# Optimization experiments

Measured on AMD Instinct MI355X. Metric: run time of the kernel, lower is better.

## Reference

```python
import jax, jax.numpy as jnp
import numpy as np

R = 2          # total_rel
N = 6144       # total_ent / num nodes
H1 = 256       # layer 1 out
H2 = 256       # layer 2 out


def setup_inputs() -> dict:
    key = jax.random.key(0)
    k_adj, k_w1, k_c1, k_w2, k_c2 = jax.random.split(key, 5)
    adj = jax.random.uniform(k_adj, (R, N, N), dtype=jnp.float32)
    bw1 = jax.random.normal(k_w1, (R, N, H1), dtype=jnp.float32) * (1.0 / np.sqrt(N))
    bc1 = jax.random.normal(k_c1, (R, R), dtype=jnp.float32)
    bw2 = jax.random.normal(k_w2, (R, H1, H2), dtype=jnp.float32) * (1.0 / np.sqrt(H1))
    bc2 = jax.random.normal(k_c2, (R, R), dtype=jnp.float32)
    return {"adj": adj, "bw1": bw1, "bc1": bc1, "bw2": bw2, "bc2": bc2}


def _layer_weights(coeff, basis):
    # (R, n_basis) x (n_basis, in, out) -> (R*in, out)
    w = jnp.einsum('ij,jmn->imn', coeff, basis)
    return w.reshape(w.shape[0] * w.shape[1], w.shape[2])


def reference(adj, bw1, bc1, bw2, bc2):
    # --- layer 1: node_init is None -> features are dense adjacencies ---
    w1 = _layer_weights(bc1, bw1)                        # (R*N, H1)
    # cat([adj[0], adj[1]], axis=1) == transpose+reshape  (N, R*N)
    tmp1 = adj.transpose(1, 0, 2).reshape(N, R * N)
    out1 = tmp1 @ w1                                     # (N, H1)

    # --- layer 2: relu then per-relation spmm + basis matmul ---
    x = jax.nn.relu(out1)
    w2 = _layer_weights(bc2, bw2)                        # (R*H1, H2)
    # cat([adj[r] @ x for r], axis=1) as one einsum       (N, R*H1)
    tmp2 = jnp.einsum('rij,jd->ird', adj, x).reshape(N, R * H1)
    out2 = tmp2 @ w2                                     # (N, H2)

    final_rep = jnp.concatenate([out1, out2], axis=1)    # (N, H1+H2)
    final_rep = jnp.sum(final_rep, axis=0).reshape(-1, H1 + H2)  # (1, H1+H2)
    return (out2, final_rep)
```

## Files before the change

### kernel.cpp

```cpp
#include <hip/hip_runtime.h>


#define NN 6144
#define HH 256
#define SPLIT 8
#define KCHUNK 1536
#define KSTEPS 24

typedef __attribute__((ext_vector_type(4))) float f32x4;
typedef __attribute__((ext_vector_type(8))) unsigned short u16x8;
typedef __attribute__((ext_vector_type(4))) unsigned short u16x4;

__device__ __forceinline__ unsigned short f2bf(float f) {
  unsigned int u = __float_as_uint(f);
  u += 0x7FFFu + ((u >> 16) & 1u);
  return (unsigned short)(u >> 16);
}
__device__ __forceinline__ float bf2f(unsigned short h) {
  return __uint_as_float(((unsigned int)h) << 16);
}

__device__ __forceinline__ void mfma_bf16(f32x4& d, u16x8 a, u16x8 b) {
  asm("v_mfma_f32_16x16x32_bf16 %0, %1, %2, %0" : "+v"(d) : "v"(a), "v"(b));
}

#define BAR_PRE_STAGE()   asm volatile("s_barrier" ::: "memory")
#define BAR_PRE_COMPUTE() asm volatile("s_waitcnt lgkmcnt(0)\n\ts_barrier" ::: "memory")

__global__ void prep_kernel(const float* __restrict__ bw1, const float* __restrict__ bc1,
                            const float* __restrict__ bw2, const float* __restrict__ bc2,
                            unsigned short* __restrict__ B1ws, unsigned short* __restrict__ w2ws,
                            float* __restrict__ fin)
{
  const int b   = blockIdx.x;
  const int tid = threadIdx.x;
  if (b >= 200) { fin[(b - 200) * 256 + tid] = 0.f; return; }

  const float* basis; const float* bc; unsigned short* outw;
  int tilesPerR, jdim, t;
  if (b < 192) { basis = bw1; bc = bc1; outw = B1ws; tilesPerR = 96; jdim = NN; t = b; }
  else         { basis = bw2; bc = bc2; outw = w2ws; tilesPerR = 4;  jdim = HH; t = b - 192; }

  __shared__ unsigned short wt[64][265];
  const int r  = t / tilesPerR;
  const int jt = t % tilesPerR;
  const float c0 = bc[r * 2 + 0];
  const float c1 = bc[r * 2 + 1];
  const float* b0 = basis + (size_t)jt * 64 * HH;
  const float* b1 = basis + (size_t)jdim * HH + (size_t)jt * 64 * HH;
#pragma unroll
  for (int k = 0; k < 16; ++k) {
    int idx = tid + k * 256;
    int row = idx >> 6;
    int c4  = (idx & 63) * 4;
    f32x4 v0 = *(const f32x4*)(b0 + (size_t)row * HH + c4);
    f32x4 v1 = *(const f32x4*)(b1 + (size_t)row * HH + c4);
    wt[row][c4 + 0] = f2bf(c0 * v0.x + c1 * v1.x);
    wt[row][c4 + 1] = f2bf(c0 * v0.y + c1 * v1.y);
    wt[row][c4 + 2] = f2bf(c0 * v0.z + c1 * v1.z);
    wt[row][c4 + 3] = f2bf(c0 * v0.w + c1 * v1.w);
  }
  __syncthreads();
#pragma unroll
  for (int k = 0; k < 8; ++k) {
    int chunk = tid + k * 256;
    int h  = chunk >> 3;
    int sp = chunk & 7;
    int j0 = (sp ^ (h & 7)) * 8;
    u16x8 v;
#pragma unroll
    for (int e = 0; e < 8; ++e) v[e] = wt[j0 + e][h];
    *(u16x8*)(outw + ((size_t)t * 2048 + chunk) * 8) = v;
  }
}

#define GEMM_PROLOGUE_COMMON()                                                 \
  const int tid  = threadIdx.x;                                                \
  const int lane = tid & 63;                                                   \
  const int wave = tid >> 6;                                                   \
  const int bid  = blockIdx.x;                                                 \
  const int s    = bid & 7;                    \
  const int mb   = bid >> 3;                                                   \
  const int i0 = mb * 64;                                                      \
  const int kbase = s * KCHUNK;                                                \
  const int tBase = kbase / 64;                                                \
  const unsigned short* bBase = Bws + (size_t)tBase * 2048 * 8 + (size_t)tid * 8;

#define DECL_ACC()                                                             \
  f32x4 acc[4][4];                                                             \
  _Pragma("unroll")                                                            \
  for (int m = 0; m < 4; ++m)                                                  \
    _Pragma("unroll")                                                          \
    for (int n = 0; n < 4; ++n) acc[m][n] = (f32x4){0.f, 0.f, 0.f, 0.f};

#define ISSUE_B(KK) do {                                                       \
    _Pragma("unroll")                                                          \
    for (int c = 0; c < 8; ++c)                                                \
      bv[c] = *(const u16x8*)(bBase + (size_t)(KK) * 2048 * 8 + c * 256 * 8);  \
  } while (0)

#define STAGE_B() do {                                                         \
    _Pragma("unroll")                                                          \
    for (int c = 0; c < 8; ++c)                                                \
      *(u16x8*)(Blds + ((size_t)c * 256 + tid) * 8) = bv[c];                   \
  } while (0)

#define COMPUTE() do {                                                         \
    _Pragma("unroll")                                                          \
    for (int ks = 0; ks < 2; ++ks) {                                           \
      u16x8 af[4], bfr[4];                                                     \
      _Pragma("unroll")                                                        \
      for (int m = 0; m < 4; ++m) {                                            \
        int row = m * 16 + (lane & 15);                                        \
        int off = (ks * 64 + ((lane >> 4) << 4)) ^ ((row & 7) << 4);           \
        af[m] = *(const u16x8*)((const char*)Alds + row * 128 + off);          \
      }                                                                        \
      _Pragma("unroll")                                                        \
      for (int n = 0; n < 4; ++n) {                                            \
        int row = wave * 64 + n * 16 + (lane & 15);                            \
        int off = (ks * 64 + ((lane >> 4) << 4)) ^ ((row & 7) << 4);           \
        bfr[n] = *(const u16x8*)((const char*)Blds + row * 128 + off);         \
      }                                                                        \
      _Pragma("unroll")                                                        \
      for (int m = 0; m < 4; ++m)                                              \
        _Pragma("unroll")                                                      \
        for (int n = 0; n < 4; ++n)                                            \
          mfma_bf16(acc[m][n], af[m], bfr[n]);                                 \
    } } while (0)

#define WRITE_P() do {                                                         \
    unsigned short* P = Pp + ((size_t)s * NN + i0) * HH;                       \
    _Pragma("unroll")                                                          \
    for (int m = 0; m < 4; ++m)                                                \
      _Pragma("unroll")                                                        \
      for (int n = 0; n < 4; ++n) {                                            \
        int col = wave * 64 + n * 16 + (lane & 15);                            \
        _Pragma("unroll")                                                      \
        for (int q = 0; q < 4; ++q) {                                          \
          int row = m * 16 + ((lane >> 4) << 2) + q;                           \
          P[(size_t)row * HH + col] = f2bf(acc[m][n][q]);                      \
        }                                                                      \
      } } while (0)

#define ISSUE_A(SET, KK) do {                                                  \
    _Pragma("unroll")                                                          \
    for (int it = 0; it < 4; ++it)                                             \
      SET[it] = *(const f32x4*)(aRow + (size_t)it * 16 * NN + (KK) * 64);      \
  } while (0)

__global__ __launch_bounds__(256, 3) void gemm_adj_store_kernel(
    const float* __restrict__ adj, const unsigned short* __restrict__ Bws,
    unsigned short* __restrict__ Pp, unsigned short* __restrict__ Aws)
{
  __shared__ __align__(16) unsigned short Alds[64 * 64];
  __shared__ __align__(16) unsigned short Blds[256 * 64];
  GEMM_PROLOGUE_COMMON();
  const int rrel = kbase / NN;
  const int jb   = kbase % NN;
  const float* aRow = adj + (size_t)rrel * NN * NN
                      + (size_t)(i0 + (tid >> 4)) * NN + jb + (tid & 15) * 4;
  char* aTile0 = (char*)Aws + ((size_t)(s * 96 + mb) * 24) * 8192;

  DECL_ACC();
  f32x4 av0[4], av1[4];
  u16x8 bv[8];

#define STAGE_A_ST(SET, KK) do {                                               \
    char* at = aTile0 + (size_t)(KK) * 8192;                                   \
    _Pragma("unroll")                                                          \
    for (int it = 0; it < 4; ++it) {                                           \
      int row = (tid >> 4) + it * 16;                                          \
      int off = ((tid & 15) * 8) ^ ((row & 7) << 4);                           \
      u16x4 w;                                                                 \
      w[0] = f2bf(SET[it].x); w[1] = f2bf(SET[it].y);                          \
      w[2] = f2bf(SET[it].z); w[3] = f2bf(SET[it].w);                          \
      *(u16x4*)((char*)Alds + row * 128 + off) = w;                            \
      *(u16x4*)(at + row * 128 + off) = w;                                     \
    } } while (0)

  ISSUE_A(av0, 0);
  ISSUE_A(av1, 1);
  ISSUE_B(0);

  for (int kk = 0; kk < KSTEPS; kk += 2) {
    BAR_PRE_STAGE();
    STAGE_A_ST(av0, kk);
    STAGE_B();
    BAR_PRE_COMPUTE();
    ISSUE_B(kk + 1);
    COMPUTE();
    BAR_PRE_STAGE();
    STAGE_A_ST(av1, kk + 1);
    STAGE_B();
    BAR_PRE_COMPUTE();
    if (kk + 2 < KSTEPS) {
      ISSUE_A(av0, kk + 2);
      ISSUE_A(av1, kk + 3);
      ISSUE_B(kk + 2);
    }
    COMPUTE();
  }
#undef STAGE_A_ST
  WRITE_P();
}

__global__ __launch_bounds__(256, 3) void gemm_adj_bf_kernel(
    const unsigned short* __restrict__ Aws, const unsigned short* __restrict__ Bws,
    unsigned short* __restrict__ Pp)
{
  __shared__ __align__(16) unsigned short Alds[64 * 64];
  __shared__ __align__(16) unsigned short Blds[256 * 64];
  GEMM_PROLOGUE_COMMON();
  const char* aTile0 = (const char*)Aws + ((size_t)(s * 96 + mb) * 24) * 8192;

  DECL_ACC();
  u16x8 av0[2], av1[2];
  u16x8 bv[8];

#define ISSUE_A2(SET, KK) do {                                                 \
    const char* at = aTile0 + (size_t)(KK) * 8192 + (size_t)tid * 32;          \
    SET[0] = *(const u16x8*)(at);                                              \
    SET[1] = *(const u16x8*)(at + 16);                                         \
  } while (0)

#define STAGE_A2(SET) do {                                                     \
    *(u16x8*)((char*)Alds + (size_t)tid * 32) = SET[0];                        \
    *(u16x8*)((char*)Alds + (size_t)tid * 32 + 16) = SET[1];                   \
  } while (0)

  ISSUE_A2(av0, 0);
  ISSUE_A2(av1, 1);
  ISSUE_B(0);

  for (int kk = 0; kk < KSTEPS; kk += 2) {
    BAR_PRE_STAGE();
    STAGE_A2(av0);
    STAGE_B();
    BAR_PRE_COMPUTE();
    ISSUE_B(kk + 1);
    COMPUTE();
    BAR_PRE_STAGE();
    STAGE_A2(av1);
    STAGE_B();
    BAR_PRE_COMPUTE();
    if (kk + 2 < KSTEPS) {
      ISSUE_A2(av0, kk + 2);
      ISSUE_A2(av1, kk + 3);
      ISSUE_B(kk + 2);
    }
    COMPUTE();
  }
#undef ISSUE_A2
#undef STAGE_A2
  WRITE_P();
}

__global__ __launch_bounds__(256, 3) void gemm_adj_kernel(
    const float* __restrict__ adj, const unsigned short* __restrict__ Bws,
    unsigned short* __restrict__ Pp)
{
  __shared__ __align__(16) unsigned short Alds[64 * 64];
  __shared__ __align__(16) unsigned short Blds[256 * 64];
  GEMM_PROLOGUE_COMMON();
  const int rrel = kbase / NN;
  const int jb   = kbase % NN;
  const float* aRow = adj + (size_t)rrel * NN * NN
                      + (size_t)(i0 + (tid >> 4)) * NN + jb + (tid & 15) * 4;

  DECL_ACC();
  f32x4 av0[4], av1[4];
  u16x8 bv[8];

#define STAGE_A(SET) do {                                                      \
    _Pragma("unroll")                                                          \
    for (int it = 0; it < 4; ++it) {                                           \
      int row = (tid >> 4) + it * 16;                                          \
      int off = ((tid & 15) * 8) ^ ((row & 7) << 4);                           \
      u16x4 w;                                                                 \
      w[0] = f2bf(SET[it].x); w[1] = f2bf(SET[it].y);                          \
      w[2] = f2bf(SET[it].z); w[3] = f2bf(SET[it].w);                          \
      *(u16x4*)((char*)Alds + row * 128 + off) = w;                            \
    } } while (0)

  ISSUE_A(av0, 0);
  ISSUE_A(av1, 1);
  ISSUE_B(0);

  for (int kk = 0; kk < KSTEPS; kk += 2) {
    BAR_PRE_STAGE();
    STAGE_A(av0);
    STAGE_B();
    BAR_PRE_COMPUTE();
    ISSUE_B(kk + 1);
    COMPUTE();
    BAR_PRE_STAGE();
    STAGE_A(av1);
    STAGE_B();
    BAR_PRE_COMPUTE();
    if (kk + 2 < KSTEPS) {
      ISSUE_A(av0, kk + 2);
      ISSUE_A(av1, kk + 3);
      ISSUE_B(kk + 2);
    }
    COMPUTE();
  }
#undef STAGE_A
  WRITE_P();
}

__global__ __launch_bounds__(256, 2) void gemm_y_kernel(
    const unsigned short* __restrict__ xws, const unsigned short* __restrict__ w2ws,
    unsigned short* __restrict__ B2ws)
{
  __shared__ __align__(16) unsigned short Alds[64 * 64];
  __shared__ __align__(16) unsigned short Blds[256 * 64];
  const int tid  = threadIdx.x;
  const int lane = tid & 63;
  const int wave = tid >> 6;
  const int mb = blockIdx.x;
  const int r  = blockIdx.y;

  f32x4 acc[4][4];
#pragma unroll
  for (int m = 0; m < 4; ++m)
#pragma unroll
    for (int n = 0; n < 4; ++n) acc[m][n] = (f32x4){0.f, 0.f, 0.f, 0.f};

  for (int dt = 0; dt < 4; ++dt) {
    u16x8 avv[2];
    avv[0] = *(const u16x8*)(xws + (((size_t)(mb * 4 + dt)) * 512 + tid) * 8);
    avv[1] = *(const u16x8*)(xws + (((size_t)(mb * 4 + dt)) * 512 + 256 + tid) * 8);
    u16x8 bv[8];
#pragma unroll
    for (int c = 0; c < 8; ++c)
      bv[c] = *(const u16x8*)(w2ws + (((size_t)(r * 4 + dt)) * 2048 + c * 256 + tid) * 8);
    __syncthreads();
    *(u16x8*)(Alds + (size_t)tid * 8) = avv[0];
    *(u16x8*)(Alds + ((size_t)256 + tid) * 8) = avv[1];
#pragma unroll
    for (int c = 0; c < 8; ++c)
      *(u16x8*)(Blds + ((size_t)c * 256 + tid) * 8) = bv[c];
    __syncthreads();
#pragma unroll
    for (int ks = 0; ks < 2; ++ks) {
      u16x8 af[4], bfr[4];
#pragma unroll
      for (int m = 0; m < 4; ++m) {
        int row = m * 16 + (lane & 15);
        int off = (ks * 64 + ((lane >> 4) << 4)) ^ ((row & 7) << 4);
        af[m] = *(const u16x8*)((const char*)Alds + row * 128 + off);
      }
#pragma unroll
      for (int n = 0; n < 4; ++n) {
        int row = wave * 64 + n * 16 + (lane & 15);
        int off = (ks * 64 + ((lane >> 4) << 4)) ^ ((row & 7) << 4);
        bfr[n] = *(const u16x8*)((const char*)Blds + row * 128 + off);
      }
#pragma unroll
      for (int m = 0; m < 4; ++m)
#pragma unroll
        for (int n = 0; n < 4; ++n)
          mfma_bf16(acc[m][n], af[m], bfr[n]);
    }
  }
  const int tg = r * 96 + mb;
#pragma unroll
  for (int m = 0; m < 4; ++m) {
    int scont = m * 2 + ((lane >> 4) >> 1);
    int e0    = ((lane >> 4) & 1) * 4;
#pragma unroll
    for (int n = 0; n < 4; ++n) {
      int h   = wave * 64 + n * 16 + (lane & 15);
      int pos = scont ^ (h & 7);
      u16x4 v;
      v[0] = f2bf(acc[m][n][0]); v[1] = f2bf(acc[m][n][1]);
      v[2] = f2bf(acc[m][n][2]); v[3] = f2bf(acc[m][n][3]);
      *(u16x4*)(B2ws + (((size_t)tg * 2048 + h * 8 + pos) * 8 + e0)) = v;
    }
  }
}

__global__ void reduce1_kernel(const unsigned short* __restrict__ Pp,
                               unsigned short* __restrict__ xws,
                               float* __restrict__ fin)
{
  __shared__ float csm[8][256];
  const int tid = threadIdx.x;
  const int b   = blockIdx.x;
  const int hc  = tid & 31;
  const int rg  = tid >> 5;
  const int dt    = hc >> 3;
  const int scont = hc & 7;
  float cs[8] = {0.f, 0.f, 0.f, 0.f, 0.f, 0.f, 0.f, 0.f};
  for (int k = 0; k < 8; ++k) {
    int i = b * 64 + rg + k * 8;
    float sv[8] = {0.f, 0.f, 0.f, 0.f, 0.f, 0.f, 0.f, 0.f};
#pragma unroll
    for (int s = 0; s < SPLIT; ++s) {
      u16x8 v = *(const u16x8*)(Pp + ((size_t)s * NN + i) * HH + hc * 8);
#pragma unroll
      for (int e = 0; e < 8; ++e) sv[e] += bf2f(v[e]);
    }
    u16x8 xv;
#pragma unroll
    for (int e = 0; e < 8; ++e) {
      cs[e] += sv[e];
      xv[e] = f2bf(fmaxf(sv[e], 0.f));
    }
    int pos = scont ^ (i & 7);
    *(u16x8*)(xws + (((size_t)(b * 4 + dt)) * 512 + (i & 63) * 8 + pos) * 8) = xv;
  }
#pragma unroll
  for (int e = 0; e < 8; ++e) csm[rg][hc * 8 + e] = cs[e];
  __syncthreads();
  float v = 0.f;
#pragma unroll
  for (int r8 = 0; r8 < 8; ++r8) v += csm[r8][tid];
  atomicAdd(&fin[tid], v);
}

__global__ void reduce2_kernel(const unsigned short* __restrict__ Pp,
                               float* __restrict__ outp,
                               float* __restrict__ fin)
{
  __shared__ float csm[8][256];
  const int tid = threadIdx.x;
  const int b   = blockIdx.x;
  const int hc  = tid & 31;
  const int rg  = tid >> 5;
  float cs[8] = {0.f, 0.f, 0.f, 0.f, 0.f, 0.f, 0.f, 0.f};
  for (int k = 0; k < 8; ++k) {
    int i = b * 64 + rg + k * 8;
    float sv[8] = {0.f, 0.f, 0.f, 0.f, 0.f, 0.f, 0.f, 0.f};
#pragma unroll
    for (int s = 0; s < SPLIT; ++s) {
      u16x8 v = *(const u16x8*)(Pp + ((size_t)s * NN + i) * HH + hc * 8);
#pragma unroll
      for (int e = 0; e < 8; ++e) sv[e] += bf2f(v[e]);
    }
    float* o = outp + (size_t)i * HH + hc * 8;
    *(f32x4*)o = (f32x4){sv[0], sv[1], sv[2], sv[3]};
    *(f32x4*)(o + 4) = (f32x4){sv[4], sv[5], sv[6], sv[7]};
#pragma unroll
    for (int e = 0; e < 8; ++e) cs[e] += sv[e];
  }
#pragma unroll
  for (int e = 0; e < 8; ++e) csm[rg][hc * 8 + e] = cs[e];
  __syncthreads();
  float v = 0.f;
#pragma unroll
  for (int r8 = 0; r8 < 8; ++r8) v += csm[r8][tid];
  atomicAdd(&fin[256 + tid], v);
}

extern "C" void kernel_launch(void* const* d_in, const int* in_sizes, int n_in,
                              void* d_out, int out_size, void* d_ws, size_t ws_size,
                              hipStream_t stream)
{
  const float* adj = (const float*)d_in[0];
  const float* bw1 = (const float*)d_in[1];
  const float* bc1 = (const float*)d_in[2];
  const float* bw2 = (const float*)d_in[3];
  const float* bc2 = (const float*)d_in[4];
  float* out2 = (float*)d_out;
  float* fin  = (float*)d_out + (size_t)NN * HH;

  char* ws = (char*)d_ws;
  unsigned short* Pp   = (unsigned short*)(ws + 0);
  unsigned short* B1ws = (unsigned short*)(ws + 25165824);
  unsigned short* B2ws = (unsigned short*)(ws + 31457280);
  unsigned short* xws  = (unsigned short*)(ws + 37748736);
  unsigned short* w2ws = (unsigned short*)(ws + 40894464);
  unsigned short* Aws  = (unsigned short*)(ws + 41943040);
  const bool handoff = (ws_size >= (size_t)192937984);

  prep_kernel<<<202, 256, 0, stream>>>(bw1, bc1, bw2, bc2, B1ws, w2ws, fin);
  if (handoff)
    gemm_adj_store_kernel<<<768, 256, 0, stream>>>(adj, B1ws, Pp, Aws);
  else
    gemm_adj_kernel<<<768, 256, 0, stream>>>(adj, B1ws, Pp);
  reduce1_kernel<<<96, 256, 0, stream>>>(Pp, xws, fin);
  gemm_y_kernel<<<dim3(96, 2), 256, 0, stream>>>(xws, w2ws, B2ws);
  if (handoff)
    gemm_adj_bf_kernel<<<768, 256, 0, stream>>>(Aws, B2ws, Pp);
  else
    gemm_adj_kernel<<<768, 256, 0, stream>>>(adj, B2ws, Pp);
  reduce2_kernel<<<96, 256, 0, stream>>>(Pp, out2, fin);
}
```

Baseline: 189.8 us.

## Load B fragments directly from global into registers, dropping B LDS staging

```diff
diff --git a/kernel.cpp b/kernel.cpp
--- a/kernel.cpp
+++ b/kernel.cpp
@@ -9,6 +9,7 @@
 
 typedef __attribute__((ext_vector_type(4))) float f32x4;
 typedef __attribute__((ext_vector_type(8))) unsigned short u16x8;
+typedef __attribute__((ext_vector_type(8))) short s16x8;
 typedef __attribute__((ext_vector_type(4))) unsigned short u16x4;
 
 __device__ __forceinline__ unsigned short f2bf(float f) {
@@ -22,6 +23,10 @@
 
 __device__ __forceinline__ void mfma_bf16(f32x4& d, u16x8 a, u16x8 b) {
   asm("v_mfma_f32_16x16x32_bf16 %0, %1, %2, %0" : "+v"(d) : "v"(a), "v"(b));
+}
+__device__ __forceinline__ void mfma_bf16b(f32x4& d, u16x8 a, u16x8 b) {
+  d = __builtin_amdgcn_mfma_f32_16x16x32_bf16(
+        __builtin_bit_cast(s16x8, a), __builtin_bit_cast(s16x8, b), d, 0, 0, 0);
 }
 
 #define BAR_PRE_STAGE()   asm volatile("s_barrier" ::: "memory")
@@ -84,7 +89,7 @@
   const int i0 = mb * 64;                                                      \
   const int kbase = s * KCHUNK;                                                \
   const int tBase = kbase / 64;                                                \
-  const unsigned short* bBase = Bws + (size_t)tBase * 2048 * 8 + (size_t)tid * 8;
+  const char* bTile0 = (const char*)Bws + ((size_t)tBase << 15);
 
 #define DECL_ACC()                                                             \
   f32x4 acc[4][4];                                                             \
@@ -93,40 +98,29 @@
     _Pragma("unroll")                                                          \
     for (int n = 0; n < 4; ++n) acc[m][n] = (f32x4){0.f, 0.f, 0.f, 0.f};
 
-#define ISSUE_B(KK) do {                                                       \
-    _Pragma("unroll")                                                          \
-    for (int c = 0; c < 8; ++c)                                                \
-      bv[c] = *(const u16x8*)(bBase + (size_t)(KK) * 2048 * 8 + c * 256 * 8);  \
+#define ISSUE_BF(SET, KS, KK) do {                                             \
+    const char* bt = bTile0 + ((size_t)(KK) << 15);                            \
+    _Pragma("unroll")                                                          \
+    for (int n = 0; n < 4; ++n) {                                              \
+      int row = wave * 64 + n * 16 + (lane & 15);                              \
+      int off = ((KS) * 64 + ((lane >> 4) << 4)) ^ ((row & 7) << 4);           \
+      SET[n] = *(const u16x8*)(bt + row * 128 + off);                          \
+    } } while (0)
+
+#define COMPUTE_HALF(KS, BSET) do {                                            \
+    u16x8 af[4];                                                               \
+    _Pragma("unroll")                                                          \
+    for (int m = 0; m < 4; ++m) {                                              \
+      int row = m * 16 + (lane & 15);                                          \
+      int off = ((KS) * 64 + ((lane >> 4) << 4)) ^ ((row & 7) << 4);           \
+      af[m] = *(const u16x8*)((const char*)Alds + row * 128 + off);            \
+    }                                                                          \
+    _Pragma("unroll")                                                          \
+    for (int m = 0; m < 4; ++m)                                                \
+      _Pragma("unroll")                                                        \
+      for (int n = 0; n < 4; ++n)                                              \
+        mfma_bf16b(acc[m][n], af[m], BSET[n]);                                 \
   } while (0)
-
-#define STAGE_B() do {                                                         \
-    _Pragma("unroll")                                                          \
-    for (int c = 0; c < 8; ++c)                                                \
-      *(u16x8*)(Blds + ((size_t)c * 256 + tid) * 8) = bv[c];                   \
-  } while (0)
-
-#define COMPUTE() do {                                                         \
-    _Pragma("unroll")                                                          \
-    for (int ks = 0; ks < 2; ++ks) {                                           \
-      u16x8 af[4], bfr[4];                                                     \
-      _Pragma("unroll")                                                        \
-      for (int m = 0; m < 4; ++m) {                                            \
-        int row = m * 16 + (lane & 15);                                        \
-        int off = (ks * 64 + ((lane >> 4) << 4)) ^ ((row & 7) << 4);           \
-        af[m] = *(const u16x8*)((const char*)Alds + row * 128 + off);          \
-      }                                                                        \
-      _Pragma("unroll")                                                        \
-      for (int n = 0; n < 4; ++n) {                                            \
-        int row = wave * 64 + n * 16 + (lane & 15);                            \
-        int off = (ks * 64 + ((lane >> 4) << 4)) ^ ((row & 7) << 4);           \
-        bfr[n] = *(const u16x8*)((const char*)Blds + row * 128 + off);         \
-      }                                                                        \
-      _Pragma("unroll")                                                        \
-      for (int m = 0; m < 4; ++m)                                              \
-        _Pragma("unroll")                                                      \
-        for (int n = 0; n < 4; ++n)                                            \
-          mfma_bf16(acc[m][n], af[m], bfr[n]);                                 \
-    } } while (0)
 
 #define WRITE_P() do {                                                         \
     unsigned short* P = Pp + ((size_t)s * NN + i0) * HH;                       \
@@ -153,7 +147,6 @@
     unsigned short* __restrict__ Pp, unsigned short* __restrict__ Aws)
 {
   __shared__ __align__(16) unsigned short Alds[64 * 64];
-  __shared__ __align__(16) unsigned short Blds[256 * 64];
   GEMM_PROLOGUE_COMMON();
   const int rrel = kbase / NN;
   const int jb   = kbase % NN;
@@ -163,7 +156,7 @@
 
   DECL_ACC();
   f32x4 av0[4], av1[4];
-  u16x8 bv[8];
+  u16x8 bf0[4], bf1[4];
 
 #define STAGE_A_ST(SET, KK) do {                                               \
     char* at = aTile0 + (size_t)(KK) * 8192;                                   \
@@ -180,25 +173,28 @@
 
   ISSUE_A(av0, 0);
   ISSUE_A(av1, 1);
-  ISSUE_B(0);
+  ISSUE_BF(bf0, 0, 0);
+  ISSUE_BF(bf1, 1, 0);
 
   for (int kk = 0; kk < KSTEPS; kk += 2) {
     BAR_PRE_STAGE();
     STAGE_A_ST(av0, kk);
-    STAGE_B();
-    BAR_PRE_COMPUTE();
-    ISSUE_B(kk + 1);
-    COMPUTE();
+    BAR_PRE_COMPUTE();
+    COMPUTE_HALF(0, bf0);
+    ISSUE_BF(bf0, 0, kk + 1);
+    COMPUTE_HALF(1, bf1);
+    ISSUE_BF(bf1, 1, kk + 1);
     BAR_PRE_STAGE();
     STAGE_A_ST(av1, kk + 1);
-    STAGE_B();
     BAR_PRE_COMPUTE();
     if (kk + 2 < KSTEPS) {
       ISSUE_A(av0, kk + 2);
       ISSUE_A(av1, kk + 3);
-      ISSUE_B(kk + 2);
-    }
-    COMPUTE();
+    }
+    COMPUTE_HALF(0, bf0);
+    if (kk + 2 < KSTEPS) ISSUE_BF(bf0, 0, kk + 2);
+    COMPUTE_HALF(1, bf1);
+    if (kk + 2 < KSTEPS) ISSUE_BF(bf1, 1, kk + 2);
   }
 #undef STAGE_A_ST
   WRITE_P();
@@ -209,13 +205,12 @@
     unsigned short* __restrict__ Pp)
 {
   __shared__ __align__(16) unsigned short Alds[64 * 64];
-  __shared__ __align__(16) unsigned short Blds[256 * 64];
   GEMM_PROLOGUE_COMMON();
   const char* aTile0 = (const char*)Aws + ((size_t)(s * 96 + mb) * 24) * 8192;
 
   DECL_ACC();
   u16x8 av0[2], av1[2];
-  u16x8 bv[8];
+  u16x8 bf0[4], bf1[4];
 
 #define ISSUE_A2(SET, KK) do {                                                 \
     const char* at = aTile0 + (size_t)(KK) * 8192 + (size_t)tid * 32;          \
@@ -230,25 +225,28 @@
 
   ISSUE_A2(av0, 0);
   ISSUE_A2(av1, 1);
-  ISSUE_B(0);
+  ISSUE_BF(bf0, 0, 0);
+  ISSUE_BF(bf1, 1, 0);
 
   for (int kk = 0; kk < KSTEPS; kk += 2) {
     BAR_PRE_STAGE();
     STAGE_A2(av0);
-    STAGE_B();
-    BAR_PRE_COMPUTE();
-    ISSUE_B(kk + 1);
-    COMPUTE();
+    BAR_PRE_COMPUTE();
+    COMPUTE_HALF(0, bf0);
+    ISSUE_BF(bf0, 0, kk + 1);
+    COMPUTE_HALF(1, bf1);
+    ISSUE_BF(bf1, 1, kk + 1);
     BAR_PRE_STAGE();
     STAGE_A2(av1);
-    STAGE_B();
     BAR_PRE_COMPUTE();
     if (kk + 2 < KSTEPS) {
       ISSUE_A2(av0, kk + 2);
       ISSUE_A2(av1, kk + 3);
-      ISSUE_B(kk + 2);
-    }
-    COMPUTE();
+    }
+    COMPUTE_HALF(0, bf0);
+    if (kk + 2 < KSTEPS) ISSUE_BF(bf0, 0, kk + 2);
+    COMPUTE_HALF(1, bf1);
+    if (kk + 2 < KSTEPS) ISSUE_BF(bf1, 1, kk + 2);
   }
 #undef ISSUE_A2
 #undef STAGE_A2
@@ -260,7 +258,6 @@
     unsigned short* __restrict__ Pp)
 {
   __shared__ __align__(16) unsigned short Alds[64 * 64];
-  __shared__ __align__(16) unsigned short Blds[256 * 64];
   GEMM_PROLOGUE_COMMON();
   const int rrel = kbase / NN;
   const int jb   = kbase % NN;
@@ -269,7 +266,7 @@
 
   DECL_ACC();
   f32x4 av0[4], av1[4];
-  u16x8 bv[8];
+  u16x8 bf0[4], bf1[4];
 
 #define STAGE_A(SET) do {                                                      \
     _Pragma("unroll")                                                          \
@@ -284,25 +281,28 @@
 
   ISSUE_A(av0, 0);
   ISSUE_A(av1, 1);
-  ISSUE_B(0);
+  ISSUE_BF(bf0, 0, 0);
+  ISSUE_BF(bf1, 1, 0);
 
   for (int kk = 0; kk < KSTEPS; kk += 2) {
     BAR_PRE_STAGE();
     STAGE_A(av0);
-    STAGE_B();
-    BAR_PRE_COMPUTE();
-    ISSUE_B(kk + 1);
-    COMPUTE();
+    BAR_PRE_COMPUTE();
+    COMPUTE_HALF(0, bf0);
+    ISSUE_BF(bf0, 0, kk + 1);
+    COMPUTE_HALF(1, bf1);
+    ISSUE_BF(bf1, 1, kk + 1);
     BAR_PRE_STAGE();
     STAGE_A(av1);
-    STAGE_B();
     BAR_PRE_COMPUTE();
     if (kk + 2 < KSTEPS) {
       ISSUE_A(av0, kk + 2);
       ISSUE_A(av1, kk + 3);
-      ISSUE_B(kk + 2);
-    }
-    COMPUTE();
+    }
+    COMPUTE_HALF(0, bf0);
+    if (kk + 2 < KSTEPS) ISSUE_BF(bf0, 0, kk + 2);
+    COMPUTE_HALF(1, bf1);
+    if (kk + 2 < KSTEPS) ISSUE_BF(bf1, 1, kk + 2);
   }
 #undef STAGE_A
   WRITE_P();
```

Result: slower. 220.3 us (+16.1%).

## Pre-swizzle layer-1 weights into MFMA fragment order and load B directly to registers

Applied to the files above, without the earlier changes.

```diff
diff --git a/kernel.cpp b/kernel.cpp
--- a/kernel.cpp
+++ b/kernel.cpp
@@ -9,6 +9,7 @@
 
 typedef __attribute__((ext_vector_type(4))) float f32x4;
 typedef __attribute__((ext_vector_type(8))) unsigned short u16x8;
+typedef __attribute__((ext_vector_type(8))) short s16x8;
 typedef __attribute__((ext_vector_type(4))) unsigned short u16x4;
 
 __device__ __forceinline__ unsigned short f2bf(float f) {
@@ -22,6 +23,10 @@
 
 __device__ __forceinline__ void mfma_bf16(f32x4& d, u16x8 a, u16x8 b) {
   asm("v_mfma_f32_16x16x32_bf16 %0, %1, %2, %0" : "+v"(d) : "v"(a), "v"(b));
+}
+__device__ __forceinline__ void mfma_bf16b(f32x4& d, u16x8 a, u16x8 b) {
+  d = __builtin_amdgcn_mfma_f32_16x16x32_bf16(
+        __builtin_bit_cast(s16x8, a), __builtin_bit_cast(s16x8, b), d, 0, 0, 0);
 }
 
 #define BAR_PRE_STAGE()   asm volatile("s_barrier" ::: "memory")
@@ -61,20 +66,37 @@
     wt[row][c4 + 3] = f2bf(c0 * v0.w + c1 * v1.w);
   }
   __syncthreads();
-#pragma unroll
-  for (int k = 0; k < 8; ++k) {
-    int chunk = tid + k * 256;
-    int h  = chunk >> 3;
-    int sp = chunk & 7;
-    int j0 = (sp ^ (h & 7)) * 8;
-    u16x8 v;
-#pragma unroll
-    for (int e = 0; e < 8; ++e) v[e] = wt[j0 + e][h];
-    *(u16x8*)(outw + ((size_t)t * 2048 + chunk) * 8) = v;
-  }
-}
-
-#define GEMM_PROLOGUE_COMMON()                                                 \
+  if (b < 192) {
+#pragma unroll
+    for (int k = 0; k < 8; ++k) {
+      int q  = tid + k * 256;
+      int l  = q & 63;
+      int n  = (q >> 6) & 3;
+      int ks = (q >> 8) & 1;
+      int w  = (q >> 9) & 3;
+      int kb = ks * 32 + ((l >> 4) << 3);
+      int h  = w * 64 + n * 16 + (l & 15);
+      u16x8 v;
+#pragma unroll
+      for (int e = 0; e < 8; ++e) v[e] = wt[kb + e][h];
+      *(u16x8*)(outw + ((size_t)t * 2048 + q) * 8) = v;
+    }
+  } else {
+#pragma unroll
+    for (int k = 0; k < 8; ++k) {
+      int chunk = tid + k * 256;
+      int h  = chunk >> 3;
+      int sp = chunk & 7;
+      int j0 = (sp ^ (h & 7)) * 8;
+      u16x8 v;
+#pragma unroll
+      for (int e = 0; e < 8; ++e) v[e] = wt[j0 + e][h];
+      *(u16x8*)(outw + ((size_t)t * 2048 + chunk) * 8) = v;
+    }
+  }
+}
+
+#define GEMM_IDX()                                                             \
   const int tid  = threadIdx.x;                                                \
   const int lane = tid & 63;                                                   \
   const int wave = tid >> 6;                                                   \
@@ -83,8 +105,7 @@
   const int mb   = bid >> 3;                                                   \
   const int i0 = mb * 64;                                                      \
   const int kbase = s * KCHUNK;                                                \
-  const int tBase = kbase / 64;                                                \
-  const unsigned short* bBase = Bws + (size_t)tBase * 2048 * 8 + (size_t)tid * 8;
+  const int tBase = kbase / 64;
 
 #define DECL_ACC()                                                             \
   f32x4 acc[4][4];                                                             \
@@ -92,41 +113,6 @@
   for (int m = 0; m < 4; ++m)                                                  \
     _Pragma("unroll")                                                          \
     for (int n = 0; n < 4; ++n) acc[m][n] = (f32x4){0.f, 0.f, 0.f, 0.f};
-
-#define ISSUE_B(KK) do {                                                       \
-    _Pragma("unroll")                                                          \
-    for (int c = 0; c < 8; ++c)                                                \
-      bv[c] = *(const u16x8*)(bBase + (size_t)(KK) * 2048 * 8 + c * 256 * 8);  \
-  } while (0)
-
-#define STAGE_B() do {                                                         \
-    _Pragma("unroll")                                                          \
-    for (int c = 0; c < 8; ++c)                                                \
-      *(u16x8*)(Blds + ((size_t)c * 256 + tid) * 8) = bv[c];                   \
-  } while (0)
-
-#define COMPUTE() do {                                                         \
-    _Pragma("unroll")                                                          \
-    for (int ks = 0; ks < 2; ++ks) {                                           \
-      u16x8 af[4], bfr[4];                                                     \
-      _Pragma("unroll")                                                        \
-      for (int m = 0; m < 4; ++m) {                                            \
-        int row = m * 16 + (lane & 15);                                        \
-        int off = (ks * 64 + ((lane >> 4) << 4)) ^ ((row & 7) << 4);           \
-        af[m] = *(const u16x8*)((const char*)Alds + row * 128 + off);          \
-      }                                                                        \
-      _Pragma("unroll")                                                        \
-      for (int n = 0; n < 4; ++n) {                                            \
-        int row = wave * 64 + n * 16 + (lane & 15);                            \
-        int off = (ks * 64 + ((lane >> 4) << 4)) ^ ((row & 7) << 4);           \
-        bfr[n] = *(const u16x8*)((const char*)Blds + row * 128 + off);         \
-      }                                                                        \
-      _Pragma("unroll")                                                        \
-      for (int m = 0; m < 4; ++m)                                              \
-        _Pragma("unroll")                                                      \
-        for (int n = 0; n < 4; ++n)                                            \
-          mfma_bf16(acc[m][n], af[m], bfr[n]);                                 \
-    } } while (0)
 
 #define WRITE_P() do {                                                         \
     unsigned short* P = Pp + ((size_t)s * NN + i0) * HH;                       \
@@ -148,24 +134,47 @@
       SET[it] = *(const f32x4*)(aRow + (size_t)it * 16 * NN + (KK) * 64);      \
   } while (0)
 
-__global__ __launch_bounds__(256, 3) void gemm_adj_store_kernel(
+#define ISSUE_BFC(SET, KS, KK) do {                                            \
+    const unsigned short* bt = bwBase + (size_t)(KK) * 2048 * 8;               \
+    _Pragma("unroll")                                                          \
+    for (int n = 0; n < 4; ++n)                                                \
+      SET[n] = *(const u16x8*)(bt + (size_t)(((KS) * 4 + n) * 64) * 8);        \
+  } while (0)
+
+#define COMPUTE_HALF(KS, BSET) do {                                            \
+    u16x8 af[4];                                                               \
+    _Pragma("unroll")                                                          \
+    for (int m = 0; m < 4; ++m) {                                              \
+      int row = m * 16 + (lane & 15);                                          \
+      int off = ((KS) * 64 + ((lane >> 4) << 4)) ^ ((row & 7) << 4);           \
+      af[m] = *(const u16x8*)((const char*)Alds + row * 128 + off);            \
+    }                                                                          \
+    _Pragma("unroll")                                                          \
+    for (int m = 0; m < 4; ++m)                                                \
+      _Pragma("unroll")                                                        \
+      for (int n = 0; n < 4; ++n)                                              \
+        mfma_bf16b(acc[m][n], af[m], BSET[n]);                                 \
+  } while (0)
+
+template <bool STORE>
+__global__ __launch_bounds__(256, 3) void gemm1_kernel(
     const float* __restrict__ adj, const unsigned short* __restrict__ Bws,
     unsigned short* __restrict__ Pp, unsigned short* __restrict__ Aws)
 {
   __shared__ __align__(16) unsigned short Alds[64 * 64];
-  __shared__ __align__(16) unsigned short Blds[256 * 64];
-  GEMM_PROLOGUE_COMMON();
+  GEMM_IDX();
   const int rrel = kbase / NN;
   const int jb   = kbase % NN;
   const float* aRow = adj + (size_t)rrel * NN * NN
                       + (size_t)(i0 + (tid >> 4)) * NN + jb + (tid & 15) * 4;
+  const unsigned short* bwBase = Bws + ((size_t)tBase * 2048 + (size_t)wave * 512 + lane) * 8;
   char* aTile0 = (char*)Aws + ((size_t)(s * 96 + mb) * 24) * 8192;
 
   DECL_ACC();
   f32x4 av0[4], av1[4];
-  u16x8 bv[8];
-
-#define STAGE_A_ST(SET, KK) do {                                               \
+  u16x8 bf0[4], bf1[4];
+
+#define STAGE_A1(SET, KK) do {                                                 \
     char* at = aTile0 + (size_t)(KK) * 8192;                                   \
     _Pragma("unroll")                                                          \
     for (int it = 0; it < 4; ++it) {                                           \
@@ -175,43 +184,47 @@
       w[0] = f2bf(SET[it].x); w[1] = f2bf(SET[it].y);                          \
       w[2] = f2bf(SET[it].z); w[3] = f2bf(SET[it].w);                          \
       *(u16x4*)((char*)Alds + row * 128 + off) = w;                            \
-      *(u16x4*)(at + row * 128 + off) = w;                                     \
+      if (STORE) *(u16x4*)(at + row * 128 + off) = w;                          \
     } } while (0)
 
   ISSUE_A(av0, 0);
   ISSUE_A(av1, 1);
-  ISSUE_B(0);
+  ISSUE_BFC(bf0, 0, 0);
+  ISSUE_BFC(bf1, 1, 0);
 
   for (int kk = 0; kk < KSTEPS; kk += 2) {
     BAR_PRE_STAGE();
-    STAGE_A_ST(av0, kk);
-    STAGE_B();
+    STAGE_A1(av0, kk);
     BAR_PRE_COMPUTE();
-    ISSUE_B(kk + 1);
-    COMPUTE();
+    COMPUTE_HALF(0, bf0);
+    ISSUE_BFC(bf0, 0, kk + 1);
+    COMPUTE_HALF(1, bf1);
+    ISSUE_BFC(bf1, 1, kk + 1);
     BAR_PRE_STAGE();
-    STAGE_A_ST(av1, kk + 1);
-    STAGE_B();
+    STAGE_A1(av1, kk + 1);
     BAR_PRE_COMPUTE();
     if (kk + 2 < KSTEPS) {
       ISSUE_A(av0, kk + 2);
       ISSUE_A(av1, kk + 3);
-      ISSUE_B(kk + 2);
-    }
-    COMPUTE();
-  }
-#undef STAGE_A_ST
+    }
+    COMPUTE_HALF(0, bf0);
+    if (kk + 2 < KSTEPS) ISSUE_BFC(bf0, 0, kk + 2);
+    COMPUTE_HALF(1, bf1);
+    if (kk + 2 < KSTEPS) ISSUE_BFC(bf1, 1, kk + 2);
+  }
+#undef STAGE_A1
   WRITE_P();
 }
 
-__global__ __launch_bounds__(256, 3) void gemm_adj_bf_kernel(
+__global__ __launch_bounds__(256, 3) void gemm2_kernel(
     const unsigned short* __restrict__ Aws, const unsigned short* __restrict__ Bws,
     unsigned short* __restrict__ Pp)
 {
   __shared__ __align__(16) unsigned short Alds[64 * 64];
   __shared__ __align__(16) unsigned short Blds[256 * 64];
-  GEMM_PROLOGUE_COMMON();
+  GEMM_IDX();
   const char* aTile0 = (const char*)Aws + ((size_t)(s * 96 + mb) * 24) * 8192;
+  const unsigned short* bBase = Bws + (size_t)tBase * 2048 * 8 + (size_t)tid * 8;
 
   DECL_ACC();
   u16x8 av0[2], av1[2];
@@ -228,50 +241,87 @@
     *(u16x8*)((char*)Alds + (size_t)tid * 32 + 16) = SET[1];                   \
   } while (0)
 
+#define ISSUE_B2(KK) do {                                                      \
+    _Pragma("unroll")                                                          \
+    for (int c = 0; c < 8; ++c)                                                \
+      bv[c] = *(const u16x8*)(bBase + (size_t)(KK) * 2048 * 8 + c * 256 * 8);  \
+  } while (0)
+
+#define STAGE_B2() do {                                                        \
+    _Pragma("unroll")                                                          \
+    for (int c = 0; c < 8; ++c)                                                \
+      *(u16x8*)(Blds + ((size_t)c * 256 + tid) * 8) = bv[c];                   \
+  } while (0)
+
+#define COMPUTE2() do {                                                        \
+    _Pragma("unroll")                                                          \
+    for (int ks = 0; ks < 2; ++ks) {                                           \
+      u16x8 af[4], bfr[4];                                                     \
+      _Pragma("unroll")                                                        \
+      for (int m = 0; m < 4; ++m) {                                            \
+        int row = m * 16 + (lane & 15);                                        \
+        int off = (ks * 64 + ((lane >> 4) << 4)) ^ ((row & 7) << 4);           \
+        af[m] = *(const u16x8*)((const char*)Alds + row * 128 + off);          \
+      }                                                                        \
+      _Pragma("unroll")                                                        \
+      for (int n = 0; n < 4; ++n) {                                            \
+        int row = wave * 64 + n * 16 + (lane & 15);                            \
+        int off = (ks * 64 + ((lane >> 4) << 4)) ^ ((row & 7) << 4);           \
+        bfr[n] = *(const u16x8*)((const char*)Blds + row * 128 + off);         \
+      }                                                                        \
+      _Pragma("unroll")                                                        \
+      for (int m = 0; m < 4; ++m)                                              \
+        _Pragma("unroll")                                                      \
+        for (int n = 0; n < 4; ++n)                                            \
+          mfma_bf16(acc[m][n], af[m], bfr[n]);                                 \
+    } } while (0)
+
   ISSUE_A2(av0, 0);
+  ISSUE_B2(0);
   ISSUE_A2(av1, 1);
-  ISSUE_B(0);
 
   for (int kk = 0; kk < KSTEPS; kk += 2) {
     BAR_PRE_STAGE();
     STAGE_A2(av0);
-    STAGE_B();
+    STAGE_B2();
     BAR_PRE_COMPUTE();
-    ISSUE_B(kk + 1);
-    COMPUTE();
+    ISSUE_B2(kk + 1);
+    if (kk + 2 < KSTEPS) ISSUE_A2(av0, kk + 2);
+    COMPUTE2();
     BAR_PRE_STAGE();
     STAGE_A2(av1);
-    STAGE_B();
+    STAGE_B2();
     BAR_PRE_COMPUTE();
-    if (kk + 2 < KSTEPS) {
-      ISSUE_A2(av0, kk + 2);
-      ISSUE_A2(av1, kk + 3);
-      ISSUE_B(kk + 2);
-    }
-    COMPUTE();
+    if (kk + 2 < KSTEPS) ISSUE_B2(kk + 2);
+    if (kk + 3 < KSTEPS) ISSUE_A2(av1, kk + 3);
+    COMPUTE2();
   }
 #undef ISSUE_A2
 #undef STAGE_A2
+#undef ISSUE_B2
+#undef STAGE_B2
+#undef COMPUTE2
   WRITE_P();
 }
 
-__global__ __launch_bounds__(256, 3) void gemm_adj_kernel(
+__global__ __launch_bounds__(256, 3) void gemm2_fp32_kernel(
     const float* __restrict__ adj, const unsigned short* __restrict__ Bws,
     unsigned short* __restrict__ Pp)
 {
   __shared__ __align__(16) unsigned short Alds[64 * 64];
   __shared__ __align__(16) unsigned short Blds[256 * 64];
-  GEMM_PROLOGUE_COMMON();
+  GEMM_IDX();
   const int rrel = kbase / NN;
   const int jb   = kbase % NN;
   const float* aRow = adj + (size_t)rrel * NN * NN
                       + (size_t)(i0 + (tid >> 4)) * NN + jb + (tid & 15) * 4;
+  const unsigned short* bBase = Bws + (size_t)tBase * 2048 * 8 + (size_t)tid * 8;
 
   DECL_ACC();
   f32x4 av0[4], av1[4];
   u16x8 bv[8];
 
-#define STAGE_A(SET) do {                                                      \
+#define STAGE_AF(SET) do {                                                     \
     _Pragma("unroll")                                                          \
     for (int it = 0; it < 4; ++it) {                                           \
       int row = (tid >> 4) + it * 16;                                          \
@@ -282,29 +332,65 @@
       *(u16x4*)((char*)Alds + row * 128 + off) = w;                            \
     } } while (0)
 
+#define ISSUE_BF2(KK) do {                                                     \
+    _Pragma("unroll")                                                          \
+    for (int c = 0; c < 8; ++c)                                                \
+      bv[c] = *(const u16x8*)(bBase + (size_t)(KK) * 2048 * 8 + c * 256 * 8);  \
+  } while (0)
+
+#define STAGE_BF2() do {                                                       \
+    _Pragma("unroll")                                                          \
+    for (int c = 0; c < 8; ++c)                                                \
+      *(u16x8*)(Blds + ((size_t)c * 256 + tid) * 8) = bv[c];                   \
+  } while (0)
+
+#define COMPUTEF() do {                                                        \
+    _Pragma("unroll")                                                          \
+    for (int ks = 0; ks < 2; ++ks) {                                           \
+      u16x8 af[4], bfr[4];                                                     \
+      _Pragma("unroll")                                                        \
+      for (int m = 0; m < 4; ++m) {                                            \
+        int row = m * 16 + (lane & 15);                                        \
+        int off = (ks * 64 + ((lane >> 4) << 4)) ^ ((row & 7) << 4);           \
+        af[m] = *(const u16x8*)((const char*)Alds + row * 128 + off);          \
+      }                                                                        \
+      _Pragma("unroll")                                                        \
+      for (int n = 0; n < 4; ++n) {                                            \
+        int row = wave * 64 + n * 16 + (lane & 15);                            \
+        int off = (ks * 64 + ((lane >> 4) << 4)) ^ ((row & 7) << 4);           \
+        bfr[n] = *(const u16x8*)((const char*)Blds + row * 128 + off);         \
+      }                                                                        \
+      _Pragma("unroll")                                                        \
+      for (int m = 0; m < 4; ++m)                                              \
+        _Pragma("unroll")                                                      \
+        for (int n = 0; n < 4; ++n)                                            \
+          mfma_bf16(acc[m][n], af[m], bfr[n]);                                 \
+    } } while (0)
+
   ISSUE_A(av0, 0);
+  ISSUE_BF2(0);
   ISSUE_A(av1, 1);
-  ISSUE_B(0);
 
   for (int kk = 0; kk < KSTEPS; kk += 2) {
     BAR_PRE_STAGE();
-    STAGE_A(av0);
-    STAGE_B();
+    STAGE_AF(av0);
+    STAGE_BF2();
     BAR_PRE_COMPUTE();
-    ISSUE_B(kk + 1);
-    COMPUTE();
+    ISSUE_BF2(kk + 1);
+    if (kk + 2 < KSTEPS) ISSUE_A(av0, kk + 2);
+    COMPUTEF();
     BAR_PRE_STAGE();
-    STAGE_A(av1);
-    STAGE_B();
+    STAGE_AF(av1);
+    STAGE_BF2();
     BAR_PRE_COMPUTE();
-    if (kk + 2 < KSTEPS) {
-      ISSUE_A(av0, kk + 2);
-      ISSUE_A(av1, kk + 3);
-      ISSUE_B(kk + 2);
-    }
-    COMPUTE();
-  }
-#undef STAGE_A
+    if (kk + 2 < KSTEPS) ISSUE_BF2(kk + 2);
+    if (kk + 3 < KSTEPS) ISSUE_A(av1, kk + 3);
+    COMPUTEF();
+  }
+#undef STAGE_AF
+#undef ISSUE_BF2
+#undef STAGE_BF2
+#undef COMPUTEF
   WRITE_P();
 }
 
@@ -475,15 +561,16 @@
   const bool handoff = (ws_size >= (size_t)192937984);
 
   prep_kernel<<<202, 256, 0, stream>>>(bw1, bc1, bw2, bc2, B1ws, w2ws, fin);
-  if (handoff)
-    gemm_adj_store_kernel<<<768, 256, 0, stream>>>(adj, B1ws, Pp, Aws);
-  else
-    gemm_adj_kernel<<<768, 256, 0, stream>>>(adj, B1ws, Pp);
-  reduce1_kernel<<<96, 256, 0, stream>>>(Pp, xws, fin);
-  gemm_y_kernel<<<dim3(96, 2), 256, 0, stream>>>(xws, w2ws, B2ws);
-  if (handoff)
-    gemm_adj_bf_kernel<<<768, 256, 0, stream>>>(Aws, B2ws, Pp);
-  else
-    gemm_adj_kernel<<<768, 256, 0, stream>>>(adj, B2ws, Pp);
+  if (handoff) {
+    gemm1_kernel<true><<<768, 256, 0, stream>>>(adj, B1ws, Pp, Aws);
+    reduce1_kernel<<<96, 256, 0, stream>>>(Pp, xws, fin);
+    gemm_y_kernel<<<dim3(96, 2), 256, 0, stream>>>(xws, w2ws, B2ws);
+    gemm2_kernel<<<768, 256, 0, stream>>>(Aws, B2ws, Pp);
+  } else {
+    gemm1_kernel<false><<<768, 256, 0, stream>>>(adj, B1ws, Pp, (unsigned short*)ws);
+    reduce1_kernel<<<96, 256, 0, stream>>>(Pp, xws, fin);
+    gemm_y_kernel<<<dim3(96, 2), 256, 0, stream>>>(xws, w2ws, B2ws);
+    gemm2_fp32_kernel<<<768, 256, 0, stream>>>(adj, B2ws, Pp);
+  }
   reduce2_kernel<<<96, 256, 0, stream>>>(Pp, out2, fin);
 }
```

Result: slower. 203.5 us (+7.2%).
